# Performance work log

Measured on AMD Instinct MI355X. Metric: run time of the kernel, lower is better.

Reference implementation:

```python
import jax, jax.numpy as jnp
import numpy as np

B, K, SD, NA = 2, 512, 60, 5
E, H, D, FF, NL = 256, 4, 64, 1024, 2
EPS_F = 1e-6   # feature_eps in phi(x)=relu(x)+eps
LN_EPS = 1e-5  # torch LayerNorm default eps


def setup_inputs() -> dict:
    key = jax.random.key(0)
    ks = jax.random.split(key, 16)
    f = lambda i, shape, s=0.02: jax.random.normal(ks[i], shape, dtype=jnp.float32) * s
    return {
        "rtg": jax.random.normal(ks[0], (B, K, 1), dtype=jnp.float32),
        "state": jax.random.normal(ks[1], (B, K, SD), dtype=jnp.float32),
        "action": jax.random.normal(ks[2], (B, K, NA), dtype=jnp.float32),
        "rtg_w": f(3, (1, E)), "rtg_b": jnp.zeros((E,), jnp.float32),
        "state_w": f(4, (SD, E)), "state_b": jnp.zeros((E,), jnp.float32),
        "action_w": f(5, (NA, E)), "action_b": jnp.zeros((E,), jnp.float32),
        "pos_emb": f(6, (K, E)),
        "norm1_g": jnp.ones((NL, E), jnp.float32), "norm1_b": jnp.zeros((NL, E), jnp.float32),
        "qkv_w": f(7, (NL, E, 3 * E)), "qkv_b": jnp.zeros((NL, 3 * E), jnp.float32),
        "out_w": f(8, (NL, E, E)), "out_b": jnp.zeros((NL, E), jnp.float32),
        "norm2_g": jnp.ones((NL, E), jnp.float32), "norm2_b": jnp.zeros((NL, E), jnp.float32),
        "ffn1_w": f(9, (NL, E, FF)), "ffn1_b": jnp.zeros((NL, FF), jnp.float32),
        "ffn2_w": f(10, (NL, FF, E)), "ffn2_b": jnp.zeros((NL, E), jnp.float32),
        "normf_g": jnp.ones((E,), jnp.float32), "normf_b": jnp.zeros((E,), jnp.float32),
        "pred_w": f(11, (E, NA)), "pred_b": jnp.zeros((NA,), jnp.float32),
    }


def _ln(x, g, b):
    m = x.mean(-1, keepdims=True)
    v = jnp.mean((x - m) ** 2, -1, keepdims=True)
    return (x - m) * jax.lax.rsqrt(v + LN_EPS) * g + b


def _attn(x, qkv_w, qkv_b, out_w, out_b):
    b, l, _ = x.shape
    qkv = (x @ qkv_w + qkv_b).reshape(b, l, 3, H, D).transpose(2, 0, 3, 1, 4)
    q, k, v = qkv[0], qkv[1], qkv[2]          # each (b,h,l,d)
    q = jax.nn.relu(q) + EPS_F
    k = jax.nn.relu(k) + EPS_F
    kv = jnp.cumsum(jnp.einsum('bhld,bhle->bhlde', k, v), axis=2)  # (b,h,l,d,e)
    kcum = jnp.cumsum(k, axis=2)
    num = jnp.einsum('bhld,bhlde->bhle', q, kv)
    den = jnp.maximum(jnp.einsum('bhld,bhld->bhl', q, kcum)[..., None], 1e-6)
    o = (num / den).transpose(0, 2, 1, 3).reshape(b, l, H * D)
    return o @ out_w + out_b


def reference(rtg, state, action, rtg_w, rtg_b, state_w, state_b, action_w, action_b,
              pos_emb, norm1_g, norm1_b, qkv_w, qkv_b, out_w, out_b,
              norm2_g, norm2_b, ffn1_w, ffn1_b, ffn2_w, ffn2_b,
              normf_g, normf_b, pred_w, pred_b):
    b, k, _ = state.shape
    p = pos_emb[:k][None]
    r = rtg @ rtg_w + rtg_b + p
    s = state @ state_w + state_b + p
    a = action @ action_w + action_b + p
    # interleave (r,s,a) per timestep -> (b, 3k, E)
    x = jnp.stack((r, s, a), axis=2).reshape(b, 3 * k, E)
    for i in range(NL):
        x = x + _attn(_ln(x, norm1_g[i], norm1_b[i]), qkv_w[i], qkv_b[i], out_w[i], out_b[i])
        h = _ln(x, norm2_g[i], norm2_b[i])
        h = jax.nn.gelu(h @ ffn1_w[i] + ffn1_b[i], approximate=False) @ ffn2_w[i] + ffn2_b[i]
        x = x + h
    x = _ln(x, normf_g, normf_b)
    return x[:, 1::3, :] @ pred_w + pred_b  # predict from state tokens -> (b,k,num_actions)
```

## Files before the change

kernel.cpp:

```cpp
#include <hip/hip_runtime.h>
#include <hip/hip_bf16.h>
#include <math.h>

#define B_  2
#define K_  512
#define SD_ 60
#define NA_ 5
#define E_  256
#define H_  4
#define D_  64
#define FF_ 1024
#define NL_ 2
#define L_  (3 * K_)
#define M_  (B_ * L_)
#define EPS_F 1e-6f
#define LN_EPS 1e-5f
#define CHK 64
#define NC_ (L_ / CHK)

using bf16x8 = __attribute__((ext_vector_type(8))) short;
using f32x4  = __attribute__((ext_vector_type(4))) float;
typedef unsigned short u16;

__device__ inline u16 f2b(float v) {
    __hip_bfloat16 h = __float2bfloat16(v);
    return *(u16*)&h;
}
__device__ inline float b2f(u16 v) {
    __hip_bfloat16 h = *(__hip_bfloat16*)&v;
    return __bfloat162float(h);
}

__global__ __launch_bounds__(256) void wconv_kernel(
    const float* __restrict__ qkv_w, const float* __restrict__ out_w,
    const float* __restrict__ ffn1_w, const float* __restrict__ ffn2_w,
    u16* __restrict__ qkvT, u16* __restrict__ outT,
    u16* __restrict__ f1T, u16* __restrict__ f2T)
{
    int tb = blockIdx.x;
    int layer = tb / 768;
    int r = tb % 768;
    const float* src; u16* dst; int K, N, tidx;
    if (r < 192)      { src = qkv_w  + layer * 196608; dst = qkvT + layer * 196608; K = 256;  N = 768;  tidx = r; }
    else if (r < 256) { src = out_w  + layer * 65536;  dst = outT + layer * 65536;  K = 256;  N = 256;  tidx = r - 192; }
    else if (r < 512) { src = ffn1_w + layer * 262144; dst = f1T  + layer * 262144; K = 256;  N = 1024; tidx = r - 256; }
    else              { src = ffn2_w + layer * 262144; dst = f2T  + layer * 262144; K = 1024; N = 256;  tidx = r - 512; }
    int tilesN = N >> 5;
    int k0 = (tidx / tilesN) << 5;
    int n0 = (tidx % tilesN) << 5;
    __shared__ u16 T[32][33];
    int c = threadIdx.x & 31, r0 = threadIdx.x >> 5;
    for (int rr = r0; rr < 32; rr += 8)
        T[rr][c] = f2b(src[(size_t)(k0 + rr) * N + n0 + c]);
    __syncthreads();
    for (int rr = r0; rr < 32; rr += 8)
        dst[(size_t)(n0 + rr) * K + k0 + c] = T[c][rr];
}

__global__ __launch_bounds__(256) void embed_ln_kernel(
    const float* __restrict__ rtg, const float* __restrict__ state,
    const float* __restrict__ action,
    const float* __restrict__ rtg_w, const float* __restrict__ rtg_b,
    const float* __restrict__ state_w, const float* __restrict__ state_b,
    const float* __restrict__ action_w, const float* __restrict__ action_b,
    const float* __restrict__ pos,
    const float* __restrict__ g, const float* __restrict__ bta,
    float* __restrict__ X, u16* __restrict__ Y)
{
    int tok = blockIdx.x * 4 + (threadIdx.x >> 6);
    int lane = threadIdx.x & 63;
    int b = tok / L_, l = tok % L_;
    int j = l % 3, t = l / 3;
    int e0 = lane * 4;
    float4 val = *(const float4*)(pos + t * E_ + e0);
    if (j == 0) {
        float rv = rtg[b * K_ + t];
        float4 w = *(const float4*)(rtg_w + e0);
        float4 bb = *(const float4*)(rtg_b + e0);
        val.x += rv * w.x + bb.x; val.y += rv * w.y + bb.y;
        val.z += rv * w.z + bb.z; val.w += rv * w.w + bb.w;
    } else if (j == 1) {
        float4 a = *(const float4*)(state_b + e0);
        const float* srow = state + ((size_t)b * K_ + t) * SD_;
        for (int i = 0; i < SD_; i++) {
            float s = srow[i];
            float4 w = *(const float4*)(state_w + (size_t)i * E_ + e0);
            a.x += s * w.x; a.y += s * w.y; a.z += s * w.z; a.w += s * w.w;
        }
        val.x += a.x; val.y += a.y; val.z += a.z; val.w += a.w;
    } else {
        float4 a = *(const float4*)(action_b + e0);
        const float* arow = action + ((size_t)b * K_ + t) * NA_;
        #pragma unroll
        for (int i = 0; i < NA_; i++) {
            float s = arow[i];
            float4 w = *(const float4*)(action_w + (size_t)i * E_ + e0);
            a.x += s * w.x; a.y += s * w.y; a.z += s * w.z; a.w += s * w.w;
        }
        val.x += a.x; val.y += a.y; val.z += a.z; val.w += a.w;
    }
    *(float4*)(X + (size_t)tok * E_ + e0) = val;
    float s = val.x + val.y + val.z + val.w;
    #pragma unroll
    for (int o = 32; o; o >>= 1) s += __shfl_xor(s, o, 64);
    float mean = s * (1.f / E_);
    float dx = val.x - mean, dy = val.y - mean, dz = val.z - mean, dw = val.w - mean;
    float q = dx * dx + dy * dy + dz * dz + dw * dw;
    #pragma unroll
    for (int o = 32; o; o >>= 1) q += __shfl_xor(q, o, 64);
    float inv = rsqrtf(q * (1.f / E_) + LN_EPS);
    float4 gv = *(const float4*)(g + e0);
    float4 bv = *(const float4*)(bta + e0);
    ushort4 u;
    u.x = f2b(dx * inv * gv.x + bv.x); u.y = f2b(dy * inv * gv.y + bv.y);
    u.z = f2b(dz * inv * gv.z + bv.z); u.w = f2b(dw * inv * gv.w + bv.w);
    *(ushort4*)(Y + (size_t)tok * E_ + e0) = u;
}

__global__ __launch_bounds__(256) void ln_kernel(
    const float* __restrict__ X, const float* __restrict__ g,
    const float* __restrict__ b, u16* __restrict__ Y)
{
    int tok = blockIdx.x * 4 + (threadIdx.x >> 6);
    int lane = threadIdx.x & 63;
    int e0 = lane * 4;
    float4 v = *(const float4*)(X + (size_t)tok * E_ + e0);
    float s = v.x + v.y + v.z + v.w;
    #pragma unroll
    for (int o = 32; o; o >>= 1) s += __shfl_xor(s, o, 64);
    float mean = s * (1.f / E_);
    float dx = v.x - mean, dy = v.y - mean, dz = v.z - mean, dw = v.w - mean;
    float q = dx * dx + dy * dy + dz * dz + dw * dw;
    #pragma unroll
    for (int o = 32; o; o >>= 1) q += __shfl_xor(q, o, 64);
    float inv = rsqrtf(q * (1.f / E_) + LN_EPS);
    float4 gv = *(const float4*)(g + e0);
    float4 bv = *(const float4*)(b + e0);
    ushort4 u;
    u.x = f2b(dx * inv * gv.x + bv.x); u.y = f2b(dy * inv * gv.y + bv.y);
    u.z = f2b(dz * inv * gv.z + bv.z); u.w = f2b(dw * inv * gv.w + bv.w);
    *(ushort4*)(Y + (size_t)tok * E_ + e0) = u;
}

template <int EPI>
__global__ __launch_bounds__(256) void mgemm(
    const u16* __restrict__ A, const u16* __restrict__ Bt,
    const float* __restrict__ bias,
    u16* __restrict__ C, int M, int N, int Kd)
{
    __shared__ __align__(16) u16 As[128 * 40];
    __shared__ __align__(16) u16 Bs[128 * 40];
    int tid = threadIdx.x;
    int bm = blockIdx.y * 128, bn = blockIdx.x * 128;
    int wave = tid >> 6, lane = tid & 63;
    int wm = (wave >> 1) * 64, wn = (wave & 1) * 64;
    int lr = lane & 15, kg = lane >> 4;

    int r0 = tid >> 2, g0 = (tid & 3) * 8;
    int r1 = (tid + 256) >> 2, g1 = (tid & 3) * 8;

    f32x4 acc[4][4] = {};

    for (int k0 = 0; k0 < Kd; k0 += 32) {
        uint4 a0 = *(const uint4*)(A + (size_t)(bm + r0) * Kd + k0 + g0);
        uint4 a1 = *(const uint4*)(A + (size_t)(bm + r1) * Kd + k0 + g1);
        uint4 b0 = *(const uint4*)(Bt + (size_t)(bn + r0) * Kd + k0 + g0);
        uint4 b1 = *(const uint4*)(Bt + (size_t)(bn + r1) * Kd + k0 + g1);
        __syncthreads();
        *(uint4*)&As[r0 * 40 + g0] = a0;
        *(uint4*)&As[r1 * 40 + g1] = a1;
        *(uint4*)&Bs[r0 * 40 + g0] = b0;
        *(uint4*)&Bs[r1 * 40 + g1] = b1;
        __syncthreads();
        bf16x8 af[4], bg[4];
        #pragma unroll
        for (int i = 0; i < 4; i++)
            af[i] = *(const bf16x8*)&As[(wm + i * 16 + lr) * 40 + kg * 8];
        #pragma unroll
        for (int j = 0; j < 4; j++)
            bg[j] = *(const bf16x8*)&Bs[(wn + j * 16 + lr) * 40 + kg * 8];
        #pragma unroll
        for (int i = 0; i < 4; i++)
            #pragma unroll
            for (int j = 0; j < 4; j++)
                acc[i][j] = __builtin_amdgcn_mfma_f32_16x16x32_bf16(
                    af[i], bg[j], acc[i][j], 0, 0, 0);
    }

    #pragma unroll
    for (int i = 0; i < 4; i++) {
        #pragma unroll
        for (int j = 0; j < 4; j++) {
            int col = bn + wn + j * 16 + lr;
            float bc = bias[col];
            #pragma unroll
            for (int r = 0; r < 4; r++) {
                int row = bm + wm + i * 16 + kg * 4 + r;
                float v = acc[i][j][r] + bc;
                if (EPI == 1) v = 0.5f * v * (1.0f + erff(v * 0.70710678118654752f));
                C[(size_t)row * N + col] = f2b(v);
            }
        }
    }
}

__global__ __launch_bounds__(256) void gemm64res(
    const u16* __restrict__ A, const u16* __restrict__ Bt,
    const float* __restrict__ bias, float* __restrict__ X, int Kd)
{
    __shared__ __align__(16) u16 As[64 * 40];
    __shared__ __align__(16) u16 Bs[64 * 40];
    int tid = threadIdx.x;
    int tile = blockIdx.x;
    int bm = (tile >> 2) * 64, bn = (tile & 3) * 64;
    int wave = tid >> 6, lane = tid & 63;
    int wm = (wave >> 1) * 32, wn = (wave & 1) * 32;
    int lr = lane & 15, kg = lane >> 4;
    int r = tid >> 2, g = (tid & 3) * 8;

    f32x4 acc[2][2] = {};
    for (int k0 = 0; k0 < Kd; k0 += 32) {
        uint4 a0 = *(const uint4*)(A + (size_t)(bm + r) * Kd + k0 + g);
        uint4 b0 = *(const uint4*)(Bt + (size_t)(bn + r) * Kd + k0 + g);
        __syncthreads();
        *(uint4*)&As[r * 40 + g] = a0;
        *(uint4*)&Bs[r * 40 + g] = b0;
        __syncthreads();
        bf16x8 af[2], bg[2];
        #pragma unroll
        for (int i = 0; i < 2; i++)
            af[i] = *(const bf16x8*)&As[(wm + i * 16 + lr) * 40 + kg * 8];
        #pragma unroll
        for (int j = 0; j < 2; j++)
            bg[j] = *(const bf16x8*)&Bs[(wn + j * 16 + lr) * 40 + kg * 8];
        #pragma unroll
        for (int i = 0; i < 2; i++)
            #pragma unroll
            for (int j = 0; j < 2; j++)
                acc[i][j] = __builtin_amdgcn_mfma_f32_16x16x32_bf16(
                    af[i], bg[j], acc[i][j], 0, 0, 0);
    }
    #pragma unroll
    for (int i = 0; i < 2; i++) {
        #pragma unroll
        for (int j = 0; j < 2; j++) {
            int col = bn + wn + j * 16 + lr;
            float bc = bias[col];
            #pragma unroll
            for (int rr = 0; rr < 4; rr++) {
                int row = bm + wm + i * 16 + kg * 4 + rr;
                float v = acc[i][j][rr] + bc + X[(size_t)row * 256 + col];
                X[(size_t)row * 256 + col] = v;
            }
        }
    }
}

__global__ __launch_bounds__(256) void chunk_sum_kernel(
    const u16* __restrict__ QKV, float* __restrict__ S, float* __restrict__ Z)
{
    int blk = blockIdx.x;
    int c = blk % NC_;
    int bh = blk / NC_;
    int h = bh % H_;
    int b = bh / H_;
    __shared__ __align__(16) u16 Kt[64 * 72];
    __shared__ __align__(16) u16 Vt[64 * 72];
    int tid = threadIdx.x;
    const size_t base = ((size_t)b * L_ + (size_t)c * CHK) * 768 + h * 64;
    for (int i = tid; i < 1024; i += 256) {
        int t = i >> 4, d4 = (i & 15) << 2;
        ushort4 k = *(const ushort4*)(QKV + base + (size_t)t * 768 + 256 + d4);
        ushort4 v = *(const ushort4*)(QKV + base + (size_t)t * 768 + 512 + d4);
        Kt[(d4 + 0) * 72 + t] = f2b(fmaxf(b2f(k.x), 0.f) + EPS_F);
        Kt[(d4 + 1) * 72 + t] = f2b(fmaxf(b2f(k.y), 0.f) + EPS_F);
        Kt[(d4 + 2) * 72 + t] = f2b(fmaxf(b2f(k.z), 0.f) + EPS_F);
        Kt[(d4 + 3) * 72 + t] = f2b(fmaxf(b2f(k.w), 0.f) + EPS_F);
        Vt[(d4 + 0) * 72 + t] = v.x;
        Vt[(d4 + 1) * 72 + t] = v.y;
        Vt[(d4 + 2) * 72 + t] = v.z;
        Vt[(d4 + 3) * 72 + t] = v.w;
    }
    __syncthreads();
    int wave = tid >> 6, lane = tid & 63;
    int lr = lane & 15, kg = lane >> 4;
    int wm = wave * 16;
    bf16x8 a0 = *(const bf16x8*)&Kt[(wm + lr) * 72 + kg * 8];
    bf16x8 a1 = *(const bf16x8*)&Kt[(wm + lr) * 72 + 32 + kg * 8];
    f32x4 acc[4] = {};
    #pragma unroll
    for (int j = 0; j < 4; j++) {
        bf16x8 b0 = *(const bf16x8*)&Vt[(j * 16 + lr) * 72 + kg * 8];
        bf16x8 b1 = *(const bf16x8*)&Vt[(j * 16 + lr) * 72 + 32 + kg * 8];
        acc[j] = __builtin_amdgcn_mfma_f32_16x16x32_bf16(a0, b0, acc[j], 0, 0, 0);
        acc[j] = __builtin_amdgcn_mfma_f32_16x16x32_bf16(a1, b1, acc[j], 0, 0, 0);
    }
    if (tid < 64) {
        float z = 0.f;
        #pragma unroll 8
        for (int t = 0; t < 64; t++) z += b2f(Kt[tid * 72 + t]);
        Z[(size_t)blk * 64 + tid] = z;
    }
    float* Sp = S + (size_t)blk * 4096;
    #pragma unroll
    for (int j = 0; j < 4; j++) {
        #pragma unroll
        for (int rr = 0; rr < 4; rr++) {
            int d = wm + kg * 4 + rr;
            int e = j * 16 + lr;
            Sp[d * 64 + e] = acc[j][rr];
        }
    }
}

__global__ __launch_bounds__(256) void chunk_out_kernel(
    const u16* __restrict__ QKV, const float* __restrict__ S,
    const float* __restrict__ Z, u16* __restrict__ O)
{
    int blk = blockIdx.x;
    int c = blk % NC_;
    int bh = blk / NC_;
    int h = bh % H_;
    int b = bh / H_;
    __shared__ __align__(16) u16 Qb[64 * 72];
    __shared__ __align__(16) u16 Kb[64 * 72];
    __shared__ __align__(16) u16 Vt[64 * 72];
    __shared__ __align__(16) u16 KVt[64 * 72];
    __shared__ __align__(16) u16 Ps[64 * 72];
    __shared__ float kzs[64];
    __shared__ float rows[64];
    __shared__ float invs[64];
    int tid = threadIdx.x;
    const size_t base = ((size_t)b * L_ + (size_t)c * CHK) * 768 + h * 64;
    const float* Sbh = S + (size_t)bh * NC_ * 4096;
    for (int i = tid; i < 1024; i += 256) {
        int t = i >> 4, d4 = (i & 15) << 2;
        ushort4 q = *(const ushort4*)(QKV + base + (size_t)t * 768 + d4);
        ushort4 k = *(const ushort4*)(QKV + base + (size_t)t * 768 + 256 + d4);
        ushort4 v = *(const ushort4*)(QKV + base + (size_t)t * 768 + 512 + d4);
        ushort4 qu, ku;
        qu.x = f2b(fmaxf(b2f(q.x), 0.f) + EPS_F); qu.y = f2b(fmaxf(b2f(q.y), 0.f) + EPS_F);
        qu.z = f2b(fmaxf(b2f(q.z), 0.f) + EPS_F); qu.w = f2b(fmaxf(b2f(q.w), 0.f) + EPS_F);
        ku.x = f2b(fmaxf(b2f(k.x), 0.f) + EPS_F); ku.y = f2b(fmaxf(b2f(k.y), 0.f) + EPS_F);
        ku.z = f2b(fmaxf(b2f(k.z), 0.f) + EPS_F); ku.w = f2b(fmaxf(b2f(k.w), 0.f) + EPS_F);
        *(ushort4*)&Qb[t * 72 + d4] = qu;
        *(ushort4*)&Kb[t * 72 + d4] = ku;
        Vt[(d4 + 0) * 72 + t] = v.x;
        Vt[(d4 + 1) * 72 + t] = v.y;
        Vt[(d4 + 2) * 72 + t] = v.z;
        Vt[(d4 + 3) * 72 + t] = v.w;
        int d = t, e4 = d4;
        float4 a = make_float4(0.f, 0.f, 0.f, 0.f);
        for (int cc = 0; cc < c; cc++) {
            float4 s4 = *(const float4*)(Sbh + (size_t)cc * 4096 + d * 64 + e4);
            a.x += s4.x; a.y += s4.y; a.z += s4.z; a.w += s4.w;
        }
        KVt[(e4 + 0) * 72 + d] = f2b(a.x);
        KVt[(e4 + 1) * 72 + d] = f2b(a.y);
        KVt[(e4 + 2) * 72 + d] = f2b(a.z);
        KVt[(e4 + 3) * 72 + d] = f2b(a.w);
    }
    if (tid < 64) {
        float z = 0.f;
        const float* Zbh = Z + (size_t)bh * NC_ * 64;
        for (int cc = 0; cc < c; cc++) z += Zbh[cc * 64 + tid];
        kzs[tid] = z;
    }
    __syncthreads();

    int wave = tid >> 6, lane = tid & 63;
    int lr = lane & 15, kg = lane >> 4;
    int wm = wave * 16;

    bf16x8 aq0 = *(const bf16x8*)&Qb[(wm + lr) * 72 + kg * 8];
    bf16x8 aq1 = *(const bf16x8*)&Qb[(wm + lr) * 72 + 32 + kg * 8];

    f32x4 accs[4] = {};
    #pragma unroll
    for (int j = 0; j < 4; j++) {
        bf16x8 b0 = *(const bf16x8*)&Kb[(j * 16 + lr) * 72 + kg * 8];
        bf16x8 b1 = *(const bf16x8*)&Kb[(j * 16 + lr) * 72 + 32 + kg * 8];
        accs[j] = __builtin_amdgcn_mfma_f32_16x16x32_bf16(aq0, b0, accs[j], 0, 0, 0);
        accs[j] = __builtin_amdgcn_mfma_f32_16x16x32_bf16(aq1, b1, accs[j], 0, 0, 0);
    }
    float rsum[4] = {0.f, 0.f, 0.f, 0.f};
    #pragma unroll
    for (int j = 0; j < 4; j++) {
        #pragma unroll
        for (int rr = 0; rr < 4; rr++) {
            int m = wm + kg * 4 + rr;
            int n = j * 16 + lr;
            float v = (n <= m) ? accs[j][rr] : 0.f;
            rsum[rr] += v;
            Ps[m * 72 + n] = f2b(v);
        }
    }
    #pragma unroll
    for (int rr = 0; rr < 4; rr++) {
        float s = rsum[rr];
        s += __shfl_xor(s, 1, 64);
        s += __shfl_xor(s, 2, 64);
        s += __shfl_xor(s, 4, 64);
        s += __shfl_xor(s, 8, 64);
        if (lr == 0) rows[wm + kg * 4 + rr] = s;
    }
    __syncthreads();

    if (tid < 64) {
        float den = rows[tid];
        float acc = 0.f;
        #pragma unroll 8
        for (int d = 0; d < 64; d++) acc += b2f(Qb[tid * 72 + d]) * kzs[d];
        invs[tid] = 1.f / fmaxf(den + acc, 1e-6f);
    }

    bf16x8 ap0 = *(const bf16x8*)&Ps[(wm + lr) * 72 + kg * 8];
    bf16x8 ap1 = *(const bf16x8*)&Ps[(wm + lr) * 72 + 32 + kg * 8];
    f32x4 accn[4] = {};
    #pragma unroll
    for (int j = 0; j < 4; j++) {
        bf16x8 b0 = *(const bf16x8*)&KVt[(j * 16 + lr) * 72 + kg * 8];
        bf16x8 b1 = *(const bf16x8*)&KVt[(j * 16 + lr) * 72 + 32 + kg * 8];
        accn[j] = __builtin_amdgcn_mfma_f32_16x16x32_bf16(aq0, b0, accn[j], 0, 0, 0);
        accn[j] = __builtin_amdgcn_mfma_f32_16x16x32_bf16(aq1, b1, accn[j], 0, 0, 0);
        bf16x8 c0 = *(const bf16x8*)&Vt[(j * 16 + lr) * 72 + kg * 8];
        bf16x8 c1 = *(const bf16x8*)&Vt[(j * 16 + lr) * 72 + 32 + kg * 8];
        accn[j] = __builtin_amdgcn_mfma_f32_16x16x32_bf16(ap0, c0, accn[j], 0, 0, 0);
        accn[j] = __builtin_amdgcn_mfma_f32_16x16x32_bf16(ap1, c1, accn[j], 0, 0, 0);
    }
    __syncthreads();

    u16* Op = O + ((size_t)b * L_ + (size_t)c * CHK) * E_ + h * 64;
    #pragma unroll
    for (int j = 0; j < 4; j++) {
        #pragma unroll
        for (int rr = 0; rr < 4; rr++) {
            int m = wm + kg * 4 + rr;
            int e = j * 16 + lr;
            Op[(size_t)m * E_ + e] = f2b(accn[j][rr] * invs[m]);
        }
    }
}

__global__ __launch_bounds__(256) void lnpred_kernel(
    const float* __restrict__ X, const float* __restrict__ g,
    const float* __restrict__ bt, const float* __restrict__ W,
    const float* __restrict__ bias, float* __restrict__ Out)
{
    int si = blockIdx.x * 4 + (threadIdx.x >> 6);
    int lane = threadIdx.x & 63;
    int b = si / K_, t = si % K_;
    size_t row = (size_t)b * L_ + 3 * t + 1;
    int e0 = lane * 4;
    float4 v = *(const float4*)(X + row * E_ + e0);
    float s = v.x + v.y + v.z + v.w;
    #pragma unroll
    for (int o = 32; o; o >>= 1) s += __shfl_xor(s, o, 64);
    float mean = s * (1.f / E_);
    float dx = v.x - mean, dy = v.y - mean, dz = v.z - mean, dw = v.w - mean;
    float q = dx * dx + dy * dy + dz * dz + dw * dw;
    #pragma unroll
    for (int o = 32; o; o >>= 1) q += __shfl_xor(q, o, 64);
    float inv = rsqrtf(q * (1.f / E_) + LN_EPS);
    float4 gv = *(const float4*)(g + e0);
    float4 bv = *(const float4*)(bt + e0);
    float y0 = dx * inv * gv.x + bv.x;
    float y1 = dy * inv * gv.y + bv.y;
    float y2 = dz * inv * gv.z + bv.z;
    float y3 = dw * inv * gv.w + bv.w;
    #pragma unroll
    for (int na = 0; na < NA_; na++) {
        float a = y0 * W[(e0 + 0) * NA_ + na] + y1 * W[(e0 + 1) * NA_ + na]
                + y2 * W[(e0 + 2) * NA_ + na] + y3 * W[(e0 + 3) * NA_ + na];
        #pragma unroll
        for (int o = 32; o; o >>= 1) a += __shfl_xor(a, o, 64);
        if (lane == 0) Out[(size_t)si * NA_ + na] = a + bias[na];
    }
}

extern "C" void kernel_launch(void* const* d_in, const int* in_sizes, int n_in,
                              void* d_out, int out_size, void* d_ws, size_t ws_size,
                              hipStream_t stream) {
    const float* rtg      = (const float*)d_in[0];
    const float* state    = (const float*)d_in[1];
    const float* action   = (const float*)d_in[2];
    const float* rtg_w    = (const float*)d_in[3];
    const float* rtg_b    = (const float*)d_in[4];
    const float* state_w  = (const float*)d_in[5];
    const float* state_b  = (const float*)d_in[6];
    const float* action_w = (const float*)d_in[7];
    const float* action_b = (const float*)d_in[8];
    const float* pos_emb  = (const float*)d_in[9];
    const float* norm1_g  = (const float*)d_in[10];
    const float* norm1_b  = (const float*)d_in[11];
    const float* qkv_w    = (const float*)d_in[12];
    const float* qkv_b    = (const float*)d_in[13];
    const float* out_w    = (const float*)d_in[14];
    const float* out_b    = (const float*)d_in[15];
    const float* norm2_g  = (const float*)d_in[16];
    const float* norm2_b  = (const float*)d_in[17];
    const float* ffn1_w   = (const float*)d_in[18];
    const float* ffn1_b   = (const float*)d_in[19];
    const float* ffn2_w   = (const float*)d_in[20];
    const float* ffn2_b   = (const float*)d_in[21];
    const float* normf_g  = (const float*)d_in[22];
    const float* normf_b  = (const float*)d_in[23];
    const float* pred_w   = (const float*)d_in[24];
    const float* pred_b   = (const float*)d_in[25];
    float* out = (float*)d_out;

    float* ws = (float*)d_ws;
    float* x    = ws;
    float* S    = x + 786432;
    float* Z    = S + 786432;
    u16*   yb   = (u16*)(Z + 12288);
    u16*   qkvb = yb + 786432;
    u16*   att  = qkvb + 2359296;
    u16*   h1   = att + 786432;
    u16*   qkvT = h1 + 3145728;
    u16*   outT = qkvT + 393216;
    u16*   f1T  = outT + 131072;
    u16*   f2T  = f1T + 524288;

    wconv_kernel<<<1536, 256, 0, stream>>>(qkv_w, out_w, ffn1_w, ffn2_w,
                                           qkvT, outT, f1T, f2T);
    embed_ln_kernel<<<M_ / 4, 256, 0, stream>>>(
        rtg, state, action, rtg_w, rtg_b, state_w, state_b,
        action_w, action_b, pos_emb, norm1_g, norm1_b, x, yb);

    for (int i = 0; i < NL_; i++) {
        mgemm<0><<<dim3(768 / 128, M_ / 128), 256, 0, stream>>>(
            yb, qkvT + (size_t)i * 196608, qkv_b + i * 768, qkvb,
            M_, 768, E_);
        chunk_sum_kernel<<<B_ * H_ * NC_, 256, 0, stream>>>(qkvb, S, Z);
        chunk_out_kernel<<<B_ * H_ * NC_, 256, 0, stream>>>(qkvb, S, Z, att);
        gemm64res<<<M_ / 64 * 4, 256, 0, stream>>>(
            att, outT + (size_t)i * 65536, out_b + i * E_, x, E_);
        ln_kernel<<<M_ / 4, 256, 0, stream>>>(
            x, norm2_g + i * E_, norm2_b + i * E_, yb);
        mgemm<1><<<dim3(FF_ / 128, M_ / 128), 256, 0, stream>>>(
            yb, f1T + (size_t)i * 262144, ffn1_b + i * FF_, h1,
            M_, FF_, E_);
        gemm64res<<<M_ / 64 * 4, 256, 0, stream>>>(
            h1, f2T + (size_t)i * 262144, ffn2_b + i * E_, x, FF_);
        if (i == 0)
            ln_kernel<<<M_ / 4, 256, 0, stream>>>(
                x, norm1_g + E_, norm1_b + E_, yb);
    }
    lnpred_kernel<<<(B_ * K_) / 4, 256, 0, stream>>>(
        x, normf_g, normf_b, pred_w, pred_b, out);
}
```

Before: 279.3 us.

## Fuse LayerNorm into GEMM prologue, merge init kernels, deepen K tiles

Drops the standalone LayerNorm kernels and the bf16 normalized-activation buffer. Each GEMM block now computes per-row mean and variance from the fp32 residual and normalizes A tiles on the fly while staging them into shared memory. The weight-conversion and embedding kernels are merged into one launch, and both GEMMs use larger K steps (64 and 128) to cut barrier count. In exchange, LN statistics are recomputed by every N-block, variance uses the E[x²]−mean² form with some precision risk, and fp32 A loads double the A read traffic.

```diff
diff --git a/kernel.cpp b/kernel.cpp
--- a/kernel.cpp
+++ b/kernel.cpp
@@ -30,44 +30,44 @@
     __hip_bfloat16 h = *(__hip_bfloat16*)&v;
     return __bfloat162float(h);
 }
-
-__global__ __launch_bounds__(256) void wconv_kernel(
+__device__ inline uint pack2(float a, float b) {
+    return (uint)f2b(a) | ((uint)f2b(b) << 16);
+}
+
+__global__ __launch_bounds__(256) void init_kernel(
     const float* __restrict__ qkv_w, const float* __restrict__ out_w,
     const float* __restrict__ ffn1_w, const float* __restrict__ ffn2_w,
     u16* __restrict__ qkvT, u16* __restrict__ outT,
-    u16* __restrict__ f1T, u16* __restrict__ f2T)
-{
-    int tb = blockIdx.x;
-    int layer = tb / 768;
-    int r = tb % 768;
-    const float* src; u16* dst; int K, N, tidx;
-    if (r < 192)      { src = qkv_w  + layer * 196608; dst = qkvT + layer * 196608; K = 256;  N = 768;  tidx = r; }
-    else if (r < 256) { src = out_w  + layer * 65536;  dst = outT + layer * 65536;  K = 256;  N = 256;  tidx = r - 192; }
-    else if (r < 512) { src = ffn1_w + layer * 262144; dst = f1T  + layer * 262144; K = 256;  N = 1024; tidx = r - 256; }
-    else              { src = ffn2_w + layer * 262144; dst = f2T  + layer * 262144; K = 1024; N = 256;  tidx = r - 512; }
-    int tilesN = N >> 5;
-    int k0 = (tidx / tilesN) << 5;
-    int n0 = (tidx % tilesN) << 5;
-    __shared__ u16 T[32][33];
-    int c = threadIdx.x & 31, r0 = threadIdx.x >> 5;
-    for (int rr = r0; rr < 32; rr += 8)
-        T[rr][c] = f2b(src[(size_t)(k0 + rr) * N + n0 + c]);
-    __syncthreads();
-    for (int rr = r0; rr < 32; rr += 8)
-        dst[(size_t)(n0 + rr) * K + k0 + c] = T[c][rr];
-}
-
-__global__ __launch_bounds__(256) void embed_ln_kernel(
+    u16* __restrict__ f1T, u16* __restrict__ f2T,
     const float* __restrict__ rtg, const float* __restrict__ state,
     const float* __restrict__ action,
     const float* __restrict__ rtg_w, const float* __restrict__ rtg_b,
     const float* __restrict__ state_w, const float* __restrict__ state_b,
     const float* __restrict__ action_w, const float* __restrict__ action_b,
-    const float* __restrict__ pos,
-    const float* __restrict__ g, const float* __restrict__ bta,
-    float* __restrict__ X, u16* __restrict__ Y)
+    const float* __restrict__ pos, float* __restrict__ X)
 {
-    int tok = blockIdx.x * 4 + (threadIdx.x >> 6);
+    __shared__ u16 T[32][33];
+    if (blockIdx.x < 1536) {
+        int tb = blockIdx.x;
+        int layer = tb / 768;
+        int r = tb % 768;
+        const float* src; u16* dst; int K, N, tidx;
+        if (r < 192)      { src = qkv_w  + layer * 196608; dst = qkvT + layer * 196608; K = 256;  N = 768;  tidx = r; }
+        else if (r < 256) { src = out_w  + layer * 65536;  dst = outT + layer * 65536;  K = 256;  N = 256;  tidx = r - 192; }
+        else if (r < 512) { src = ffn1_w + layer * 262144; dst = f1T  + layer * 262144; K = 256;  N = 1024; tidx = r - 256; }
+        else              { src = ffn2_w + layer * 262144; dst = f2T  + layer * 262144; K = 1024; N = 256;  tidx = r - 512; }
+        int tilesN = N >> 5;
+        int k0 = (tidx / tilesN) << 5;
+        int n0 = (tidx % tilesN) << 5;
+        int c = threadIdx.x & 31, r0 = threadIdx.x >> 5;
+        for (int rr = r0; rr < 32; rr += 8)
+            T[rr][c] = f2b(src[(size_t)(k0 + rr) * N + n0 + c]);
+        __syncthreads();
+        for (int rr = r0; rr < 32; rr += 8)
+            dst[(size_t)(n0 + rr) * K + k0 + c] = T[c][rr];
+        return;
+    }
+    int tok = (blockIdx.x - 1536) * 4 + (threadIdx.x >> 6);
     int lane = threadIdx.x & 63;
     int b = tok / L_, l = tok % L_;
     int j = l % 3, t = l / 3;
@@ -100,91 +100,99 @@
         val.x += a.x; val.y += a.y; val.z += a.z; val.w += a.w;
     }
     *(float4*)(X + (size_t)tok * E_ + e0) = val;
-    float s = val.x + val.y + val.z + val.w;
-    #pragma unroll
-    for (int o = 32; o; o >>= 1) s += __shfl_xor(s, o, 64);
-    float mean = s * (1.f / E_);
-    float dx = val.x - mean, dy = val.y - mean, dz = val.z - mean, dw = val.w - mean;
-    float q = dx * dx + dy * dy + dz * dz + dw * dw;
-    #pragma unroll
-    for (int o = 32; o; o >>= 1) q += __shfl_xor(q, o, 64);
-    float inv = rsqrtf(q * (1.f / E_) + LN_EPS);
-    float4 gv = *(const float4*)(g + e0);
-    float4 bv = *(const float4*)(bta + e0);
-    ushort4 u;
-    u.x = f2b(dx * inv * gv.x + bv.x); u.y = f2b(dy * inv * gv.y + bv.y);
-    u.z = f2b(dz * inv * gv.z + bv.z); u.w = f2b(dw * inv * gv.w + bv.w);
-    *(ushort4*)(Y + (size_t)tok * E_ + e0) = u;
-}
-
-__global__ __launch_bounds__(256) void ln_kernel(
+}
+
+template <int EPI>
+__global__ __launch_bounds__(256) void mgemm_ln(
     const float* __restrict__ X, const float* __restrict__ g,
-    const float* __restrict__ b, u16* __restrict__ Y)
+    const float* __restrict__ bta, const u16* __restrict__ Bt,
+    const float* __restrict__ bias, u16* __restrict__ C, int N)
 {
-    int tok = blockIdx.x * 4 + (threadIdx.x >> 6);
-    int lane = threadIdx.x & 63;
-    int e0 = lane * 4;
-    float4 v = *(const float4*)(X + (size_t)tok * E_ + e0);
-    float s = v.x + v.y + v.z + v.w;
-    #pragma unroll
-    for (int o = 32; o; o >>= 1) s += __shfl_xor(s, o, 64);
-    float mean = s * (1.f / E_);
-    float dx = v.x - mean, dy = v.y - mean, dz = v.z - mean, dw = v.w - mean;
-    float q = dx * dx + dy * dy + dz * dz + dw * dw;
-    #pragma unroll
-    for (int o = 32; o; o >>= 1) q += __shfl_xor(q, o, 64);
-    float inv = rsqrtf(q * (1.f / E_) + LN_EPS);
-    float4 gv = *(const float4*)(g + e0);
-    float4 bv = *(const float4*)(b + e0);
-    ushort4 u;
-    u.x = f2b(dx * inv * gv.x + bv.x); u.y = f2b(dy * inv * gv.y + bv.y);
-    u.z = f2b(dz * inv * gv.z + bv.z); u.w = f2b(dw * inv * gv.w + bv.w);
-    *(ushort4*)(Y + (size_t)tok * E_ + e0) = u;
-}
-
-template <int EPI>
-__global__ __launch_bounds__(256) void mgemm(
-    const u16* __restrict__ A, const u16* __restrict__ Bt,
-    const float* __restrict__ bias,
-    u16* __restrict__ C, int M, int N, int Kd)
-{
-    __shared__ __align__(16) u16 As[128 * 40];
-    __shared__ __align__(16) u16 Bs[128 * 40];
+    __shared__ __align__(16) u16 As[128 * 72];
+    __shared__ __align__(16) u16 Bs[128 * 72];
+    __shared__ float meanL[128], invL[128];
+    __shared__ float sg[256], sb[256];
     int tid = threadIdx.x;
     int bm = blockIdx.y * 128, bn = blockIdx.x * 128;
     int wave = tid >> 6, lane = tid & 63;
     int wm = (wave >> 1) * 64, wn = (wave & 1) * 64;
     int lr = lane & 15, kg = lane >> 4;
 
-    int r0 = tid >> 2, g0 = (tid & 3) * 8;
-    int r1 = (tid + 256) >> 2, g1 = (tid & 3) * 8;
+    sg[tid] = g[tid];
+    sb[tid] = bta[tid];
+
+    {
+        int r = tid >> 1, hh = (tid & 1) * 128;
+        const float* xr = X + (size_t)(bm + r) * 256 + hh;
+        float s = 0.f, sq = 0.f;
+        #pragma unroll
+        for (int i = 0; i < 32; i++) {
+            float4 v = *(const float4*)(xr + i * 4);
+            s += v.x + v.y + v.z + v.w;
+            sq += v.x * v.x + v.y * v.y + v.z * v.z + v.w * v.w;
+        }
+        s += __shfl_xor(s, 1, 64);
+        sq += __shfl_xor(sq, 1, 64);
+        if ((tid & 1) == 0) {
+            float mean = s * (1.f / 256.f);
+            float var = sq * (1.f / 256.f) - mean * mean;
+            meanL[r] = mean;
+            invL[r] = rsqrtf(var + LN_EPS);
+        }
+    }
+    __syncthreads();
+
+    int ra = tid >> 1, kha = (tid & 1) * 32;
+    int rb = tid >> 1, khb = (tid & 1) * 32;
 
     f32x4 acc[4][4] = {};
 
-    for (int k0 = 0; k0 < Kd; k0 += 32) {
-        uint4 a0 = *(const uint4*)(A + (size_t)(bm + r0) * Kd + k0 + g0);
-        uint4 a1 = *(const uint4*)(A + (size_t)(bm + r1) * Kd + k0 + g1);
-        uint4 b0 = *(const uint4*)(Bt + (size_t)(bn + r0) * Kd + k0 + g0);
-        uint4 b1 = *(const uint4*)(Bt + (size_t)(bn + r1) * Kd + k0 + g1);
+    for (int k0 = 0; k0 < 256; k0 += 64) {
+        float4 av[8];
+        #pragma unroll
+        for (int s = 0; s < 8; s++)
+            av[s] = *(const float4*)(X + (size_t)(bm + ra) * 256 + k0 + kha + s * 4);
+        uint4 bv[4];
+        #pragma unroll
+        for (int s = 0; s < 4; s++)
+            bv[s] = *(const uint4*)(Bt + (size_t)(bn + rb) * 256 + k0 + khb + s * 8);
         __syncthreads();
-        *(uint4*)&As[r0 * 40 + g0] = a0;
-        *(uint4*)&As[r1 * 40 + g1] = a1;
-        *(uint4*)&Bs[r0 * 40 + g0] = b0;
-        *(uint4*)&Bs[r1 * 40 + g1] = b1;
+        float mean = meanL[ra], inv = invL[ra];
+        #pragma unroll
+        for (int s = 0; s < 4; s++) {
+            float4 v0 = av[2 * s], v1 = av[2 * s + 1];
+            int cb = k0 + kha + s * 8;
+            float4 g0 = *(const float4*)(sg + cb);
+            float4 g1 = *(const float4*)(sg + cb + 4);
+            float4 b0 = *(const float4*)(sb + cb);
+            float4 b1 = *(const float4*)(sb + cb + 4);
+            uint4 o;
+            o.x = pack2((v0.x - mean) * inv * g0.x + b0.x, (v0.y - mean) * inv * g0.y + b0.y);
+            o.y = pack2((v0.z - mean) * inv * g0.z + b0.z, (v0.w - mean) * inv * g0.w + b0.w);
+            o.z = pack2((v1.x - mean) * inv * g1.x + b1.x, (v1.y - mean) * inv * g1.y + b1.y);
+            o.w = pack2((v1.z - mean) * inv * g1.z + b1.z, (v1.w - mean) * inv * g1.w + b1.w);
+            *(uint4*)&As[ra * 72 + kha + s * 8] = o;
+        }
+        #pragma unroll
+        for (int s = 0; s < 4; s++)
+            *(uint4*)&Bs[rb * 72 + khb + s * 8] = bv[s];
         __syncthreads();
-        bf16x8 af[4], bg[4];
-        #pragma unroll
-        for (int i = 0; i < 4; i++)
-            af[i] = *(const bf16x8*)&As[(wm + i * 16 + lr) * 40 + kg * 8];
-        #pragma unroll
-        for (int j = 0; j < 4; j++)
-            bg[j] = *(const bf16x8*)&Bs[(wn + j * 16 + lr) * 40 + kg * 8];
-        #pragma unroll
-        for (int i = 0; i < 4; i++)
+        #pragma unroll
+        for (int sub = 0; sub < 64; sub += 32) {
+            bf16x8 af[4], bg[4];
+            #pragma unroll
+            for (int i = 0; i < 4; i++)
+                af[i] = *(const bf16x8*)&As[(wm + i * 16 + lr) * 72 + sub + kg * 8];
             #pragma unroll
             for (int j = 0; j < 4; j++)
-                acc[i][j] = __builtin_amdgcn_mfma_f32_16x16x32_bf16(
-                    af[i], bg[j], acc[i][j], 0, 0, 0);
+                bg[j] = *(const bf16x8*)&Bs[(wn + j * 16 + lr) * 72 + sub + kg * 8];
+            #pragma unroll
+            for (int i = 0; i < 4; i++)
+                #pragma unroll
+                for (int j = 0; j < 4; j++)
+                    acc[i][j] = __builtin_amdgcn_mfma_f32_16x16x32_bf16(
+                        af[i], bg[j], acc[i][j], 0, 0, 0);
+        }
     }
 
     #pragma unroll
@@ -208,37 +216,47 @@
     const u16* __restrict__ A, const u16* __restrict__ Bt,
     const float* __restrict__ bias, float* __restrict__ X, int Kd)
 {
-    __shared__ __align__(16) u16 As[64 * 40];
-    __shared__ __align__(16) u16 Bs[64 * 40];
+    __shared__ __align__(16) u16 As[64 * 136];
+    __shared__ __align__(16) u16 Bs[64 * 136];
     int tid = threadIdx.x;
     int tile = blockIdx.x;
     int bm = (tile >> 2) * 64, bn = (tile & 3) * 64;
     int wave = tid >> 6, lane = tid & 63;
     int wm = (wave >> 1) * 32, wn = (wave & 1) * 32;
     int lr = lane & 15, kg = lane >> 4;
-    int r = tid >> 2, g = (tid & 3) * 8;
+    int r = tid >> 2, ks = (tid & 3) * 32;
 
     f32x4 acc[2][2] = {};
-    for (int k0 = 0; k0 < Kd; k0 += 32) {
-        uint4 a0 = *(const uint4*)(A + (size_t)(bm + r) * Kd + k0 + g);
-        uint4 b0 = *(const uint4*)(Bt + (size_t)(bn + r) * Kd + k0 + g);
+    for (int k0 = 0; k0 < Kd; k0 += 128) {
+        uint4 av[4], bv[4];
+        #pragma unroll
+        for (int s = 0; s < 4; s++) {
+            av[s] = *(const uint4*)(A + (size_t)(bm + r) * Kd + k0 + ks + s * 8);
+            bv[s] = *(const uint4*)(Bt + (size_t)(bn + r) * Kd + k0 + ks + s * 8);
+        }
         __syncthreads();
-        *(uint4*)&As[r * 40 + g] = a0;
-        *(uint4*)&Bs[r * 40 + g] = b0;
+        #pragma unroll
+        for (int s = 0; s < 4; s++) {
+            *(uint4*)&As[r * 136 + ks + s * 8] = av[s];
+            *(uint4*)&Bs[r * 136 + ks + s * 8] = bv[s];
+        }
         __syncthreads();
-        bf16x8 af[2], bg[2];
-        #pragma unroll
-        for (int i = 0; i < 2; i++)
-            af[i] = *(const bf16x8*)&As[(wm + i * 16 + lr) * 40 + kg * 8];
-        #pragma unroll
-        for (int j = 0; j < 2; j++)
-            bg[j] = *(const bf16x8*)&Bs[(wn + j * 16 + lr) * 40 + kg * 8];
-        #pragma unroll
-        for (int i = 0; i < 2; i++)
+        #pragma unroll
+        for (int sub = 0; sub < 128; sub += 32) {
+            bf16x8 af[2], bg[2];
+            #pragma unroll
+            for (int i = 0; i < 2; i++)
+                af[i] = *(const bf16x8*)&As[(wm + i * 16 + lr) * 136 + sub + kg * 8];
             #pragma unroll
             for (int j = 0; j < 2; j++)
-                acc[i][j] = __builtin_amdgcn_mfma_f32_16x16x32_bf16(
-                    af[i], bg[j], acc[i][j], 0, 0, 0);
+                bg[j] = *(const bf16x8*)&Bs[(wn + j * 16 + lr) * 136 + sub + kg * 8];
+            #pragma unroll
+            for (int i = 0; i < 2; i++)
+                #pragma unroll
+                for (int j = 0; j < 2; j++)
+                    acc[i][j] = __builtin_amdgcn_mfma_f32_16x16x32_bf16(
+                        af[i], bg[j], acc[i][j], 0, 0, 0);
+        }
     }
     #pragma unroll
     for (int i = 0; i < 2; i++) {
@@ -513,8 +531,7 @@
     float* x    = ws;
     float* S    = x + 786432;
     float* Z    = S + 786432;
-    u16*   yb   = (u16*)(Z + 12288);
-    u16*   qkvb = yb + 786432;
+    u16*   qkvb = (u16*)(Z + 12288);
     u16*   att  = qkvb + 2359296;
     u16*   h1   = att + 786432;
     u16*   qkvT = h1 + 3145728;
@@ -522,30 +539,24 @@
     u16*   f1T  = outT + 131072;
     u16*   f2T  = f1T + 524288;
 
-    wconv_kernel<<<1536, 256, 0, stream>>>(qkv_w, out_w, ffn1_w, ffn2_w,
-                                           qkvT, outT, f1T, f2T);
-    embed_ln_kernel<<<M_ / 4, 256, 0, stream>>>(
+    init_kernel<<<2304, 256, 0, stream>>>(
+        qkv_w, out_w, ffn1_w, ffn2_w, qkvT, outT, f1T, f2T,
         rtg, state, action, rtg_w, rtg_b, state_w, state_b,
-        action_w, action_b, pos_emb, norm1_g, norm1_b, x, yb);
+        action_w, action_b, pos_emb, x);
 
     for (int i = 0; i < NL_; i++) {
-        mgemm<0><<<dim3(768 / 128, M_ / 128), 256, 0, stream>>>(
-            yb, qkvT + (size_t)i * 196608, qkv_b + i * 768, qkvb,
-            M_, 768, E_);
+        mgemm_ln<0><<<dim3(768 / 128, M_ / 128), 256, 0, stream>>>(
+            x, norm1_g + i * E_, norm1_b + i * E_,
+            qkvT + (size_t)i * 196608, qkv_b + i * 768, qkvb, 768);
         chunk_sum_kernel<<<B_ * H_ * NC_, 256, 0, stream>>>(qkvb, S, Z);
         chunk_out_kernel<<<B_ * H_ * NC_, 256, 0, stream>>>(qkvb, S, Z, att);
         gemm64res<<<M_ / 64 * 4, 256, 0, stream>>>(
             att, outT + (size_t)i * 65536, out_b + i * E_, x, E_);
-        ln_kernel<<<M_ / 4, 256, 0, stream>>>(
-            x, norm2_g + i * E_, norm2_b + i * E_, yb);
-        mgemm<1><<<dim3(FF_ / 128, M_ / 128), 256, 0, stream>>>(
-            yb, f1T + (size_t)i * 262144, ffn1_b + i * FF_, h1,
-            M_, FF_, E_);
+        mgemm_ln<1><<<dim3(FF_ / 128, M_ / 128), 256, 0, stream>>>(
+            x, norm2_g + i * E_, norm2_b + i * E_,
+            f1T + (size_t)i * 262144, ffn1_b + i * FF_, h1, FF_);
         gemm64res<<<M_ / 64 * 4, 256, 0, stream>>>(
             h1, f2T + (size_t)i * 262144, ffn2_b + i * E_, x, FF_);
-        if (i == 0)
-            ln_kernel<<<M_ / 4, 256, 0, stream>>>(
-                x, norm1_g + E_, norm1_b + E_, yb);
     }
     lnpred_kernel<<<(B_ * K_) / 4, 256, 0, stream>>>(
         x, normf_g, normf_b, pred_w, pred_b, out);
```

New measurement: 327.3 us. +17.2%, slower.

## Fuse LayerNorm into residual GEMMs with full-row tiles; merge weight conversion and embed

Applied to the files above, without the earlier changes.

The residual-add GEMMs now use 16-row by 256-column tiles so each block owns whole rows. That lets the following LayerNorm be computed in the epilogue, with the mean and variance reduced across waves through shared memory, and the separate ln_kernel launches disappear. The weight transpose/convert kernel and the embedding+LN kernel are merged into one launch split by block index. This trades launch count and an extra read of X for more B-tile loading per block: every block reloads the full 256-wide weight slice for only 16 rows. Variance is now computed as E[x^2]-mean^2 in one pass, which is slightly less numerically robust.

```diff
diff --git a/kernel.cpp b/kernel.cpp
--- a/kernel.cpp
+++ b/kernel.cpp
@@ -31,33 +31,11 @@
     return __bfloat162float(h);
 }
 
-__global__ __launch_bounds__(256) void wconv_kernel(
+__global__ __launch_bounds__(256) void init_kernel(
     const float* __restrict__ qkv_w, const float* __restrict__ out_w,
     const float* __restrict__ ffn1_w, const float* __restrict__ ffn2_w,
     u16* __restrict__ qkvT, u16* __restrict__ outT,
-    u16* __restrict__ f1T, u16* __restrict__ f2T)
-{
-    int tb = blockIdx.x;
-    int layer = tb / 768;
-    int r = tb % 768;
-    const float* src; u16* dst; int K, N, tidx;
-    if (r < 192)      { src = qkv_w  + layer * 196608; dst = qkvT + layer * 196608; K = 256;  N = 768;  tidx = r; }
-    else if (r < 256) { src = out_w  + layer * 65536;  dst = outT + layer * 65536;  K = 256;  N = 256;  tidx = r - 192; }
-    else if (r < 512) { src = ffn1_w + layer * 262144; dst = f1T  + layer * 262144; K = 256;  N = 1024; tidx = r - 256; }
-    else              { src = ffn2_w + layer * 262144; dst = f2T  + layer * 262144; K = 1024; N = 256;  tidx = r - 512; }
-    int tilesN = N >> 5;
-    int k0 = (tidx / tilesN) << 5;
-    int n0 = (tidx % tilesN) << 5;
-    __shared__ u16 T[32][33];
-    int c = threadIdx.x & 31, r0 = threadIdx.x >> 5;
-    for (int rr = r0; rr < 32; rr += 8)
-        T[rr][c] = f2b(src[(size_t)(k0 + rr) * N + n0 + c]);
-    __syncthreads();
-    for (int rr = r0; rr < 32; rr += 8)
-        dst[(size_t)(n0 + rr) * K + k0 + c] = T[c][rr];
-}
-
-__global__ __launch_bounds__(256) void embed_ln_kernel(
+    u16* __restrict__ f1T, u16* __restrict__ f2T,
     const float* __restrict__ rtg, const float* __restrict__ state,
     const float* __restrict__ action,
     const float* __restrict__ rtg_w, const float* __restrict__ rtg_b,
@@ -67,7 +45,28 @@
     const float* __restrict__ g, const float* __restrict__ bta,
     float* __restrict__ X, u16* __restrict__ Y)
 {
-    int tok = blockIdx.x * 4 + (threadIdx.x >> 6);
+    __shared__ u16 T[32][33];
+    if (blockIdx.x < 1536) {
+        int tb = blockIdx.x;
+        int layer = tb / 768;
+        int r = tb % 768;
+        const float* src; u16* dst; int K, N, tidx;
+        if (r < 192)      { src = qkv_w  + layer * 196608; dst = qkvT + layer * 196608; K = 256;  N = 768;  tidx = r; }
+        else if (r < 256) { src = out_w  + layer * 65536;  dst = outT + layer * 65536;  K = 256;  N = 256;  tidx = r - 192; }
+        else if (r < 512) { src = ffn1_w + layer * 262144; dst = f1T  + layer * 262144; K = 256;  N = 1024; tidx = r - 256; }
+        else              { src = ffn2_w + layer * 262144; dst = f2T  + layer * 262144; K = 1024; N = 256;  tidx = r - 512; }
+        int tilesN = N >> 5;
+        int k0 = (tidx / tilesN) << 5;
+        int n0 = (tidx % tilesN) << 5;
+        int c = threadIdx.x & 31, r0 = threadIdx.x >> 5;
+        for (int rr = r0; rr < 32; rr += 8)
+            T[rr][c] = f2b(src[(size_t)(k0 + rr) * N + n0 + c]);
+        __syncthreads();
+        for (int rr = r0; rr < 32; rr += 8)
+            dst[(size_t)(n0 + rr) * K + k0 + c] = T[c][rr];
+        return;
+    }
+    int tok = (blockIdx.x - 1536) * 4 + (threadIdx.x >> 6);
     int lane = threadIdx.x & 63;
     int b = tok / L_, l = tok % L_;
     int j = l % 3, t = l / 3;
@@ -117,31 +116,6 @@
     *(ushort4*)(Y + (size_t)tok * E_ + e0) = u;
 }
 
-__global__ __launch_bounds__(256) void ln_kernel(
-    const float* __restrict__ X, const float* __restrict__ g,
-    const float* __restrict__ b, u16* __restrict__ Y)
-{
-    int tok = blockIdx.x * 4 + (threadIdx.x >> 6);
-    int lane = threadIdx.x & 63;
-    int e0 = lane * 4;
-    float4 v = *(const float4*)(X + (size_t)tok * E_ + e0);
-    float s = v.x + v.y + v.z + v.w;
-    #pragma unroll
-    for (int o = 32; o; o >>= 1) s += __shfl_xor(s, o, 64);
-    float mean = s * (1.f / E_);
-    float dx = v.x - mean, dy = v.y - mean, dz = v.z - mean, dw = v.w - mean;
-    float q = dx * dx + dy * dy + dz * dz + dw * dw;
-    #pragma unroll
-    for (int o = 32; o; o >>= 1) q += __shfl_xor(q, o, 64);
-    float inv = rsqrtf(q * (1.f / E_) + LN_EPS);
-    float4 gv = *(const float4*)(g + e0);
-    float4 bv = *(const float4*)(b + e0);
-    ushort4 u;
-    u.x = f2b(dx * inv * gv.x + bv.x); u.y = f2b(dy * inv * gv.y + bv.y);
-    u.z = f2b(dz * inv * gv.z + bv.z); u.w = f2b(dw * inv * gv.w + bv.w);
-    *(ushort4*)(Y + (size_t)tok * E_ + e0) = u;
-}
-
 template <int EPI>
 __global__ __launch_bounds__(256) void mgemm(
     const u16* __restrict__ A, const u16* __restrict__ Bt,
@@ -204,53 +178,107 @@
     }
 }
 
-__global__ __launch_bounds__(256) void gemm64res(
+template <int DOLN>
+__global__ __launch_bounds__(256) void growln(
     const u16* __restrict__ A, const u16* __restrict__ Bt,
-    const float* __restrict__ bias, float* __restrict__ X, int Kd)
+    const float* __restrict__ bias,
+    const float* __restrict__ g, const float* __restrict__ bta,
+    float* __restrict__ X, u16* __restrict__ Y, int Kd)
 {
-    __shared__ __align__(16) u16 As[64 * 40];
-    __shared__ __align__(16) u16 Bs[64 * 40];
+    __shared__ __align__(16) u16 As[16 * 72];
+    __shared__ __align__(16) u16 Bs[256 * 72];
+    __shared__ float redS[16][4], redQ[16][4];
+    __shared__ float meanL[16], invL[16];
     int tid = threadIdx.x;
-    int tile = blockIdx.x;
-    int bm = (tile >> 2) * 64, bn = (tile & 3) * 64;
+    int bm = blockIdx.x * 16;
     int wave = tid >> 6, lane = tid & 63;
-    int wm = (wave >> 1) * 32, wn = (wave & 1) * 32;
+    int wn = wave * 64;
     int lr = lane & 15, kg = lane >> 4;
-    int r = tid >> 2, g = (tid & 3) * 8;
-
-    f32x4 acc[2][2] = {};
-    for (int k0 = 0; k0 < Kd; k0 += 32) {
-        uint4 a0 = *(const uint4*)(A + (size_t)(bm + r) * Kd + k0 + g);
-        uint4 b0 = *(const uint4*)(Bt + (size_t)(bn + r) * Kd + k0 + g);
-        __syncthreads();
-        *(uint4*)&As[r * 40 + g] = a0;
-        *(uint4*)&Bs[r * 40 + g] = b0;
-        __syncthreads();
-        bf16x8 af[2], bg[2];
-        #pragma unroll
-        for (int i = 0; i < 2; i++)
-            af[i] = *(const bf16x8*)&As[(wm + i * 16 + lr) * 40 + kg * 8];
-        #pragma unroll
-        for (int j = 0; j < 2; j++)
-            bg[j] = *(const bf16x8*)&Bs[(wn + j * 16 + lr) * 40 + kg * 8];
-        #pragma unroll
-        for (int i = 0; i < 2; i++)
+
+    f32x4 acc[4] = {};
+    for (int k0 = 0; k0 < Kd; k0 += 64) {
+        uint4 bv[8];
+        #pragma unroll
+        for (int s = 0; s < 8; s++) {
+            int seg = tid + 256 * s;
+            int rr = seg >> 3, koff = (seg & 7) * 8;
+            bv[s] = *(const uint4*)(Bt + (size_t)rr * Kd + k0 + koff);
+        }
+        uint4 av;
+        if (tid < 128) {
+            int rr = tid >> 3, koff = (tid & 7) * 8;
+            av = *(const uint4*)(A + (size_t)(bm + rr) * Kd + k0 + koff);
+        }
+        __syncthreads();
+        if (tid < 128) {
+            int rr = tid >> 3, koff = (tid & 7) * 8;
+            *(uint4*)&As[rr * 72 + koff] = av;
+        }
+        #pragma unroll
+        for (int s = 0; s < 8; s++) {
+            int seg = tid + 256 * s;
+            int rr = seg >> 3, koff = (seg & 7) * 8;
+            *(uint4*)&Bs[rr * 72 + koff] = bv[s];
+        }
+        __syncthreads();
+        #pragma unroll
+        for (int sub = 0; sub < 64; sub += 32) {
+            bf16x8 af = *(const bf16x8*)&As[lr * 72 + sub + kg * 8];
             #pragma unroll
-            for (int j = 0; j < 2; j++)
-                acc[i][j] = __builtin_amdgcn_mfma_f32_16x16x32_bf16(
-                    af[i], bg[j], acc[i][j], 0, 0, 0);
-    }
-    #pragma unroll
-    for (int i = 0; i < 2; i++) {
-        #pragma unroll
-        for (int j = 0; j < 2; j++) {
-            int col = bn + wn + j * 16 + lr;
-            float bc = bias[col];
+            for (int j = 0; j < 4; j++) {
+                bf16x8 bg = *(const bf16x8*)&Bs[(wn + j * 16 + lr) * 72 + sub + kg * 8];
+                acc[j] = __builtin_amdgcn_mfma_f32_16x16x32_bf16(af, bg, acc[j], 0, 0, 0);
+            }
+        }
+    }
+
+    float vres[4][4];
+    float rowsum[4] = {}, rowsq[4] = {};
+    #pragma unroll
+    for (int j = 0; j < 4; j++) {
+        int col = wn + j * 16 + lr;
+        float bc = bias[col];
+        #pragma unroll
+        for (int r = 0; r < 4; r++) {
+            int row = bm + kg * 4 + r;
+            float v = acc[j][r] + bc + X[(size_t)row * 256 + col];
+            X[(size_t)row * 256 + col] = v;
+            vres[j][r] = v;
+            rowsum[r] += v;
+            rowsq[r] += v * v;
+        }
+    }
+    if (DOLN) {
+        #pragma unroll
+        for (int r = 0; r < 4; r++) {
+            float a = rowsum[r], b = rowsq[r];
             #pragma unroll
-            for (int rr = 0; rr < 4; rr++) {
-                int row = bm + wm + i * 16 + kg * 4 + rr;
-                float v = acc[i][j][rr] + bc + X[(size_t)row * 256 + col];
-                X[(size_t)row * 256 + col] = v;
+            for (int o = 1; o < 16; o <<= 1) {
+                a += __shfl_xor(a, o, 64);
+                b += __shfl_xor(b, o, 64);
+            }
+            if (lr == 0) { redS[kg * 4 + r][wave] = a; redQ[kg * 4 + r][wave] = b; }
+        }
+        __syncthreads();
+        if (tid < 16) {
+            float a = redS[tid][0] + redS[tid][1] + redS[tid][2] + redS[tid][3];
+            float b = redQ[tid][0] + redQ[tid][1] + redQ[tid][2] + redQ[tid][3];
+            float mean = a * (1.f / 256.f);
+            float var = b * (1.f / 256.f) - mean * mean;
+            meanL[tid] = mean;
+            invL[tid] = rsqrtf(var + LN_EPS);
+        }
+        __syncthreads();
+        #pragma unroll
+        for (int j = 0; j < 4; j++) {
+            int col = wn + j * 16 + lr;
+            float gg = g[col], bb = bta[col];
+            #pragma unroll
+            for (int r = 0; r < 4; r++) {
+                int rloc = kg * 4 + r;
+                int row = bm + rloc;
+                Y[(size_t)row * 256 + col] =
+                    f2b((vres[j][r] - meanL[rloc]) * invL[rloc] * gg + bb);
             }
         }
     }
@@ -522,9 +550,8 @@
     u16*   f1T  = outT + 131072;
     u16*   f2T  = f1T + 524288;
 
-    wconv_kernel<<<1536, 256, 0, stream>>>(qkv_w, out_w, ffn1_w, ffn2_w,
-                                           qkvT, outT, f1T, f2T);
-    embed_ln_kernel<<<M_ / 4, 256, 0, stream>>>(
+    init_kernel<<<2304, 256, 0, stream>>>(
+        qkv_w, out_w, ffn1_w, ffn2_w, qkvT, outT, f1T, f2T,
         rtg, state, action, rtg_w, rtg_b, state_w, state_b,
         action_w, action_b, pos_emb, norm1_g, norm1_b, x, yb);
 
@@ -534,18 +561,20 @@
             M_, 768, E_);
         chunk_sum_kernel<<<B_ * H_ * NC_, 256, 0, stream>>>(qkvb, S, Z);
         chunk_out_kernel<<<B_ * H_ * NC_, 256, 0, stream>>>(qkvb, S, Z, att);
-        gemm64res<<<M_ / 64 * 4, 256, 0, stream>>>(
-            att, outT + (size_t)i * 65536, out_b + i * E_, x, E_);
-        ln_kernel<<<M_ / 4, 256, 0, stream>>>(
-            x, norm2_g + i * E_, norm2_b + i * E_, yb);
+        growln<1><<<M_ / 16, 256, 0, stream>>>(
+            att, outT + (size_t)i * 65536, out_b + i * E_,
+            norm2_g + i * E_, norm2_b + i * E_, x, yb, E_);
         mgemm<1><<<dim3(FF_ / 128, M_ / 128), 256, 0, stream>>>(
             yb, f1T + (size_t)i * 262144, ffn1_b + i * FF_, h1,
             M_, FF_, E_);
-        gemm64res<<<M_ / 64 * 4, 256, 0, stream>>>(
-            h1, f2T + (size_t)i * 262144, ffn2_b + i * E_, x, FF_);
         if (i == 0)
-            ln_kernel<<<M_ / 4, 256, 0, stream>>>(
-                x, norm1_g + E_, norm1_b + E_, yb);
+            growln<1><<<M_ / 16, 256, 0, stream>>>(
+                h1, f2T + (size_t)i * 262144, ffn2_b + i * E_,
+                norm1_g + E_, norm1_b + E_, x, yb, FF_);
+        else
+            growln<0><<<M_ / 16, 256, 0, stream>>>(
+                h1, f2T + (size_t)i * 262144, ffn2_b + i * E_,
+                nullptr, nullptr, x, nullptr, FF_);
     }
     lnpred_kernel<<<(B_ * K_) / 4, 256, 0, stream>>>(
         x, normf_g, normf_b, pred_w, pred_b, out);
```

Result: slower. 351.3 us (+25.8%).
